# Performance work log

Hardware: AMD Instinct MI355X
Metric: run time of the kernel (lower is better)

## Reference

```python
import jax, jax.numpy as jnp
import numpy as np

D_MODEL = 1024


def pos_encoding(seq_len, d_model):
    # pos: [S,1], i: [d/2]
    pos = jnp.arange(seq_len, dtype=jnp.float32)[:, None]
    i = jnp.arange(0, d_model, 2, dtype=jnp.float32)
    angle_rates = 1.0 / jnp.power(10000.0, i / d_model)
    angle_rads = pos * angle_rates  # [S, d/2]
    # NOTE: original concatenates sin block then cos block (not interleaved)
    return jnp.concatenate([jnp.sin(angle_rads), jnp.cos(angle_rads)], axis=-1)  # [S, d]


def setup_inputs() -> dict:
    key = jax.random.key(0)
    ks = jax.random.split(key, 4)
    B, S, D = 4, 2048, D_MODEL
    scale = 1.0 / np.sqrt(D)
    x = jax.random.normal(ks[0], (B, S, D), dtype=jnp.float32)
    Wq = jax.random.normal(ks[1], (D, D), dtype=jnp.float32) * scale
    Wk = jax.random.normal(ks[2], (D, D), dtype=jnp.float32) * scale
    Wv = jax.random.normal(ks[3], (D, D), dtype=jnp.float32) * scale
    bq = jnp.zeros((D,), dtype=jnp.float32)
    bk = jnp.zeros((D,), dtype=jnp.float32)
    bv = jnp.zeros((D,), dtype=jnp.float32)
    return {"x": x, "Wq": Wq, "bq": bq, "Wk": Wk, "bk": bk, "Wv": Wv, "bv": bv}


def reference(x, Wq, bq, Wk, bk, Wv, bv):
    B, S, D = x.shape
    pe = pos_encoding(S, D)  # [S, D]
    h = x + pe[None, :, :]
    q = jnp.einsum('bsd,de->bse', h, Wq) + bq
    k = jnp.einsum('bsd,de->bse', h, Wk) + bk
    v = jnp.einsum('bsd,de->bse', h, Wv) + bv
    logits = jnp.einsum('bqd,bkd->bqk', q, k) / jnp.sqrt(jnp.float32(D))
    attn = jax.nn.softmax(logits, axis=-1)
    out = jnp.einsum('bqk,bkd->bqd', attn, v)
    return x + out
```

## Files before the change

kernel.cpp:

```cpp
#include <hip/hip_runtime.h>
#include <stdint.h>


#define AS1(p) ((__attribute__((address_space(1))) void*)(p))
#define AS3(p) ((__attribute__((address_space(3))) void*)(p))

typedef _Float16 f16x8 __attribute__((ext_vector_type(8)));
typedef _Float16 f16x4 __attribute__((ext_vector_type(4)));
typedef float f32x4 __attribute__((ext_vector_type(4)));

__global__ __launch_bounds__(256) void prep(const float* __restrict__ x,
                                            _Float16* __restrict__ h,
                                            const float* __restrict__ Wq,
                                            const float* __restrict__ Wk,
                                            const float* __restrict__ Wv,
                                            _Float16* __restrict__ Wt,
                                            float* __restrict__ rowsum) {
  const int bx = blockIdx.x;
  const int tid = threadIdx.x;
  if (bx < 8192) {
    const size_t e = ((size_t)bx * 256 + tid) * 4;
    const int d = (int)(e & 1023);
    const int s = (int)((e >> 10) & 2047);
    const float4 xv = *(const float4*)(x + e);
    const int half = d >> 9;
    const int j0 = d & 511;
    const float c = -0.017988946039016f;
    f16x4 o;
#pragma unroll
    for (int t = 0; t < 4; t++) {
      const float r = __expf((float)(j0 + t) * c);
      const float a = (float)s * r;
      const float p = half ? __cosf(a) : __sinf(a);
      const float xe = (t == 0) ? xv.x : (t == 1) ? xv.y : (t == 2) ? xv.z : xv.w;
      o[t] = (_Float16)(xe + p);
    }
    *(f16x4*)(h + e) = o;
  } else if (bx < 11264) {
    __shared__ float t[32][33];
    const int w = bx - 8192;
    const int z = w >> 10;
    const int rem = w & 1023;
    const int n0 = (rem & 31) * 32, k0 = (rem >> 5) * 32;
    const float* W = (z == 0) ? Wq : (z == 1) ? Wk : Wv;
    _Float16* o = Wt + (size_t)z * 1048576;
    const int tx = tid & 31, ty = tid >> 5;
#pragma unroll
    for (int i = ty; i < 32; i += 8)
      t[i][tx] = W[(size_t)(k0 + i) * 1024 + (n0 + tx)];
    __syncthreads();
#pragma unroll
    for (int i = ty; i < 32; i += 8)
      o[(size_t)(n0 + i) * 1024 + (k0 + tx)] = (_Float16)t[tx][i];
  } else {
    rowsum[(bx - 11264) * 256 + tid] = 0.f;
  }
}

template <int MODE>
__global__ __launch_bounds__(512) void gemm8p(
    const _Float16* __restrict__ A0, long long sA,
    const _Float16* __restrict__ B0, long long sB,
    void* __restrict__ C0, long long sC,
    const float* __restrict__ aux0, const float* __restrict__ aux1,
    const float* __restrict__ aux2, float* __restrict__ rowsum,
    _Float16* __restrict__ vT, const int K, const int N, const int ldc) {
  __shared__ __align__(16) _Float16 As[2][2][8192];
  __shared__ __align__(16) _Float16 Bs[2][2][8192];
  const int tid = threadIdx.x;
  const int bid = blockIdx.x;

  int z, bm0, bn0;
  if (MODE == 0) {
    const int w = (bid & 7) * 48 + (bid >> 3);
    const int m = w / 12, r = w - m * 12;
    z = r >> 2; bn0 = (r & 3) * 256; bm0 = m * 256;
  } else {
    const int w = (bid & 7) * 32 + (bid >> 3);
    z = w >> 6;
    const int r = w & 63;
    bm0 = (r >> 3) * 256; bn0 = (r & 7) * 256;
  }
  const _Float16* A = A0 + (size_t)z * sA;
  const _Float16* Bt = B0 + (size_t)z * sB;

  const _Float16* aS = A + (size_t)(bm0 + (tid >> 2)) * K + (tid & 3) * 8;
  const _Float16* bS = Bt + (size_t)(bn0 + (tid >> 2)) * K + (tid & 3) * 8;
  const size_t half = (size_t)128 * K;

  auto stage = [&](int kt, int q) {
    const int b = kt & 1;
    _Float16* ad = &As[b][q][tid * 8];
    _Float16* bd = &Bs[b][q][tid * 8];
    const _Float16* ag = aS + kt * 64 + q * 32;
    const _Float16* bg = bS + kt * 64 + q * 32;
    __builtin_amdgcn_global_load_lds(AS1(ag), AS3(ad), 16, 0, 0);
    __builtin_amdgcn_global_load_lds(AS1(ag + half), AS3(ad + 4096), 16, 0, 0);
    __builtin_amdgcn_global_load_lds(AS1(bg), AS3(bd), 16, 0, 0);
    __builtin_amdgcn_global_load_lds(AS1(bg + half), AS3(bd + 4096), 16, 0, 0);
  };

  const int lane = tid & 63, wave = tid >> 6;
  const int wr = wave >> 2, wc = wave & 3;
  const int quad = lane >> 4, l16 = lane & 15;

  f32x4 acc[8][4];
#pragma unroll
  for (int i = 0; i < 8; i++)
#pragma unroll
    for (int j = 0; j < 4; j++) {
      f32x4 zz = {0.f, 0.f, 0.f, 0.f};
      acc[i][j] = zz;
    }

  const int nt = K >> 6;

  stage(0, 0); stage(0, 1); stage(1, 0);
  asm volatile("s_waitcnt vmcnt(8)" ::: "memory");
  __builtin_amdgcn_s_barrier();

  for (int t = 0; t < nt; ++t) {
    const int b = t & 1;
#pragma unroll
    for (int q = 0; q < 2; ++q) {
      f16x8 af[8], bf[4];
#pragma unroll
      for (int i = 0; i < 8; i++)
        af[i] = *(const f16x8*)&As[b][q][(wr * 128 + i * 16 + l16) * 32 + quad * 8];
#pragma unroll
      for (int j = 0; j < 4; j++)
        bf[j] = *(const f16x8*)&Bs[b][q][(wc * 64 + j * 16 + l16) * 32 + quad * 8];
      if (q == 0) { if (t + 1 < nt) stage(t + 1, 1); }
      else        { if (t + 2 < nt) stage(t + 2, 0); }
      __builtin_amdgcn_s_barrier();
      asm volatile("s_waitcnt lgkmcnt(0)" ::: "memory");
      __builtin_amdgcn_sched_barrier(0);
      __builtin_amdgcn_s_setprio(1);
#pragma unroll
      for (int i = 0; i < 8; i++)
#pragma unroll
        for (int j = 0; j < 4; j++)
          acc[i][j] = __builtin_amdgcn_mfma_f32_16x16x32_f16(af[i], bf[j],
                                                             acc[i][j], 0, 0, 0);
      __builtin_amdgcn_s_setprio(0);
      __builtin_amdgcn_sched_barrier(0);
      const bool last = (t == nt - 1) && (q == 1);
      if (!last) {
        if (q == 0) {
          if (t + 1 < nt) asm volatile("s_waitcnt vmcnt(8)" ::: "memory");
          else            asm volatile("s_waitcnt vmcnt(0)" ::: "memory");
        } else {
          if (t + 3 <= nt) asm volatile("s_waitcnt vmcnt(8)" ::: "memory");
          else             asm volatile("s_waitcnt vmcnt(4)" ::: "memory");
        }
        __builtin_amdgcn_s_barrier();
      }
    }
  }

  const int rowb = bm0 + wr * 128 + quad * 4;
  const int colb = bn0 + wc * 64 + l16;
  if (MODE == 0) {
    const float* bias = (z == 0) ? aux0 : (z == 1) ? aux1 : aux2;
    if (z == 2) {
      const int bb_ = rowb >> 11, sl = rowb & 2047;
      _Float16* vb = vT + (size_t)bb_ * 2097152;
#pragma unroll
      for (int i = 0; i < 8; i++)
#pragma unroll
        for (int j = 0; j < 4; j++) {
          const int gn = colb + j * 16;
          const float bb = bias[gn];
          f16x4 o;
#pragma unroll
          for (int r = 0; r < 4; r++) o[r] = (_Float16)(acc[i][j][r] + bb);
          *(f16x4*)&vb[(size_t)gn * 2048 + sl + i * 16] = o;
        }
    } else {
      _Float16* C = (_Float16*)C0 + (size_t)z * sC;
#pragma unroll
      for (int i = 0; i < 8; i++)
#pragma unroll
        for (int j = 0; j < 4; j++) {
          const int gn = colb + j * 16;
          const float bb = bias[gn];
#pragma unroll
          for (int r = 0; r < 4; r++)
            C[(size_t)(rowb + i * 16 + r) * N + gn] = (_Float16)(acc[i][j][r] + bb);
        }
    }
  } else {
    _Float16* C = (_Float16*)C0 + (size_t)z * sC;
    float rs[4] = {0.f, 0.f, 0.f, 0.f};
#pragma unroll
    for (int i = 0; i < 8; i++)
#pragma unroll
      for (int j = 0; j < 4; j++) {
        const int gn = colb + j * 16;
        f16x4 o;
        float pj = 0.f;
#pragma unroll
        for (int r = 0; r < 4; r++) {
          const float e = __expf(acc[i][j][r] * 0.03125f);
          o[r] = (_Float16)e;
          pj += e;
        }
        rs[j] += pj;
        *(f16x4*)&C[(size_t)gn * ldc + rowb + i * 16] = o;
      }
#pragma unroll
    for (int j = 0; j < 4; j++) {
      float v = rs[j];
      v += __shfl_xor(v, 16);
      v += __shfl_xor(v, 32);
      if (quad == 0) atomicAdd(&rowsum[z * 2048 + colb + j * 16], v);
    }
  }
}

__global__ __launch_bounds__(256) void gemm_pv(
    const _Float16* __restrict__ A0, long long sA,
    const _Float16* __restrict__ B0, long long sB,
    float* __restrict__ C0, long long sC,
    const float* __restrict__ X0, const float* __restrict__ rowsum,
    long long sX, const int K, const int ldc) {
  __shared__ __align__(16) _Float16 As[2 * 128 * 32];
  __shared__ __align__(16) _Float16 Bs[2 * 128 * 32];
  const int tid = threadIdx.x;
  const int bid = blockIdx.x;

  const int c = bid & 7, t0 = bid >> 3;
  const int zx = (t0 & 3) * 8 + c;
  const int y = t0 >> 2;
  const int z = zx >> 3;
  const int bm0 = (zx & 7) * 128, bn0 = y * 128;

  const _Float16* A = A0 + (size_t)z * sA;
  const _Float16* Bt = B0 + (size_t)z * sB;

  const _Float16* a0 = A + (size_t)(bm0 + (tid >> 2)) * K + (tid & 3) * 8;
  const _Float16* a1 = a0 + (size_t)64 * K;
  const _Float16* b0 = Bt + (size_t)(bn0 + (tid >> 2)) * K + (tid & 3) * 8;
  const _Float16* b1 = b0 + (size_t)64 * K;

  const int lane = tid & 63, wave = tid >> 6;
  const int wr = wave >> 1, wc = wave & 1;
  const int quad = lane >> 4, l16 = lane & 15;

  f32x4 acc[4][4];
#pragma unroll
  for (int i = 0; i < 4; i++)
#pragma unroll
    for (int j = 0; j < 4; j++) {
      f32x4 zz = {0.f, 0.f, 0.f, 0.f};
      acc[i][j] = zz;
    }

  for (int k0 = 0; k0 < K; k0 += 64) {
    __syncthreads();
#pragma unroll
    for (int u = 0; u < 2; u++) {
      __builtin_amdgcn_global_load_lds(AS1(a0 + k0 + u * 32),
                                       AS3(&As[u * 4096 + tid * 8]), 16, 0, 0);
      __builtin_amdgcn_global_load_lds(AS1(a1 + k0 + u * 32),
                                       AS3(&As[u * 4096 + tid * 8 + 2048]), 16, 0, 0);
      __builtin_amdgcn_global_load_lds(AS1(b0 + k0 + u * 32),
                                       AS3(&Bs[u * 4096 + tid * 8]), 16, 0, 0);
      __builtin_amdgcn_global_load_lds(AS1(b1 + k0 + u * 32),
                                       AS3(&Bs[u * 4096 + tid * 8 + 2048]), 16, 0, 0);
    }
    __syncthreads();
#pragma unroll
    for (int u = 0; u < 2; u++) {
      f16x8 af[4], bfr[4];
#pragma unroll
      for (int i = 0; i < 4; i++)
        af[i] = *(const f16x8*)&As[u * 4096 + (wr * 64 + i * 16 + l16) * 32 + quad * 8];
#pragma unroll
      for (int j = 0; j < 4; j++)
        bfr[j] = *(const f16x8*)&Bs[u * 4096 + (wc * 64 + j * 16 + l16) * 32 + quad * 8];
#pragma unroll
      for (int i = 0; i < 4; i++)
#pragma unroll
        for (int j = 0; j < 4; j++)
          acc[i][j] = __builtin_amdgcn_mfma_f32_16x16x32_f16(af[i], bfr[j],
                                                             acc[i][j], 0, 0, 0);
    }
  }

  const int rowb = bm0 + wr * 64 + quad * 4;
  const int colb = bn0 + wc * 64 + l16;
  float* C = C0 + (size_t)z * sC;
  const float* X = X0 + (size_t)z * sX;
  float inv[4];
#pragma unroll
  for (int j = 0; j < 4; j++)
    inv[j] = 1.0f / rowsum[z * 2048 + colb + j * 16];
#pragma unroll
  for (int i = 0; i < 4; i++)
#pragma unroll
    for (int j = 0; j < 4; j++) {
      const int gn = colb + j * 16;
      const size_t base = (size_t)gn * ldc + rowb + i * 16;
      const float4 xv = *(const float4*)(X + base);
      float4 o;
      o.x = acc[i][j][0] * inv[j] + xv.x;
      o.y = acc[i][j][1] * inv[j] + xv.y;
      o.z = acc[i][j][2] * inv[j] + xv.z;
      o.w = acc[i][j][3] * inv[j] + xv.w;
      *(float4*)(C + base) = o;
    }
}

extern "C" void kernel_launch(void* const* d_in, const int* in_sizes, int n_in,
                              void* d_out, int out_size, void* d_ws, size_t ws_size,
                              hipStream_t stream) {
  (void)in_sizes; (void)n_in; (void)out_size; (void)ws_size;
  const float* x  = (const float*)d_in[0];
  const float* Wq = (const float*)d_in[1];
  const float* bq = (const float*)d_in[2];
  const float* Wk = (const float*)d_in[3];
  const float* bk = (const float*)d_in[4];
  const float* Wv = (const float*)d_in[5];
  const float* bv = (const float*)d_in[6];
  float* out = (float*)d_out;
  char* ws = (char*)d_ws;

  _Float16* h    = (_Float16*)(ws);
  _Float16* Wt   = (_Float16*)(ws + 16777216);
  _Float16* qkv  = (_Float16*)(ws + 23068672);
  _Float16* attn = (_Float16*)(ws + 73400320);
  float* rowsum  = (float*)   (ws + 106954752);

  const long long E = 8388608;
  _Float16* vT = qkv + 2 * E;

  prep<<<11296, 256, 0, stream>>>(x, h, Wq, Wk, Wv, Wt, rowsum);

  gemm8p<0><<<384, 512, 0, stream>>>(
      h, 0LL, Wt, 1048576LL, qkv, E, bq, bk, bv, nullptr, vT,
      1024, 1024, 0);

  gemm8p<1><<<256, 512, 0, stream>>>(
      qkv + E, 2097152LL, qkv, 2097152LL, attn, 4194304LL,
      nullptr, nullptr, nullptr, rowsum, nullptr,
      1024, 2048, 2048);

  gemm_pv<<<512, 256, 0, stream>>>(
      vT, 2097152LL, attn, 4194304LL, out, 2097152LL,
      x, rowsum, 2097152LL, 2048, 1024);
}
```

Measured before the change: 271.8 us.

## Restructure GEMM main loops into finer-grained staged pipelines with quadrant MFMA phases

The 256x256 GEMM now loads full 64-wide K tiles per A/B half and splits each K step into four quadrant phases. Each phase issues a slice of the next prefetch between LDS fragment reads and MFMA bursts, so global loads are spread more evenly over the compute. The PV GEMM swaps its synchronous load-then-compute loop for a 4-slot ring buffer of 32-wide K stages, prefetched three stages ahead with vmcnt-based waits. This costs more LDS in the PV kernel and adds extra barriers per iteration in the main GEMM.

```diff
diff --git a/kernel.cpp b/kernel.cpp
--- a/kernel.cpp
+++ b/kernel.cpp
@@ -57,8 +57,39 @@
   }
 }
 
+#define RD_A(SET, S_)                                                         \
+  {                                                                           \
+    _Pragma("unroll") for (int fi = 0; fi < 4; fi++)                          \
+      _Pragma("unroll") for (int kk = 0; kk < 2; kk++)                        \
+        SET[fi * 2 + kk] = *(const f16x8*)&As[bb][kk][                        \
+            (wr * 128 + (S_) * 64 + fi * 16 + l16) * 32 + quad * 8];          \
+  }
+#define RD_B(SET, S_)                                                         \
+  {                                                                           \
+    _Pragma("unroll") for (int fj = 0; fj < 2; fj++)                          \
+      _Pragma("unroll") for (int kk = 0; kk < 2; kk++)                        \
+        SET[fj * 2 + kk] = *(const f16x8*)&Bs[bb][kk][                        \
+            (wc * 64 + (S_) * 32 + fj * 16 + l16) * 32 + quad * 8];           \
+  }
+#define MFMA16(ASET, BSET, MQ, NQ)                                            \
+  {                                                                           \
+    __builtin_amdgcn_s_setprio(1);                                            \
+    _Pragma("unroll") for (int fi = 0; fi < 4; fi++)                          \
+      _Pragma("unroll") for (int fj = 0; fj < 2; fj++)                        \
+        _Pragma("unroll") for (int kk = 0; kk < 2; kk++)                      \
+          acc[(MQ) * 4 + fi][(NQ) * 2 + fj] =                                 \
+              __builtin_amdgcn_mfma_f32_16x16x32_f16(                         \
+                  ASET[fi * 2 + kk], BSET[fj * 2 + kk],                       \
+                  acc[(MQ) * 4 + fi][(NQ) * 2 + fj], 0, 0, 0);                \
+    __builtin_amdgcn_s_setprio(0);                                            \
+  }
+#define PHASE_WAIT()                                                          \
+  __builtin_amdgcn_s_barrier();                                               \
+  asm volatile("s_waitcnt lgkmcnt(0)" ::: "memory");                          \
+  __builtin_amdgcn_sched_barrier(0);
+
 template <int MODE>
-__global__ __launch_bounds__(512) void gemm8p(
+__global__ __launch_bounds__(512) void gemm256(
     const _Float16* __restrict__ A0, long long sA,
     const _Float16* __restrict__ B0, long long sB,
     void* __restrict__ C0, long long sC,
@@ -86,18 +117,21 @@
 
   const _Float16* aS = A + (size_t)(bm0 + (tid >> 2)) * K + (tid & 3) * 8;
   const _Float16* bS = Bt + (size_t)(bn0 + (tid >> 2)) * K + (tid & 3) * 8;
-  const size_t half = (size_t)128 * K;
-
-  auto stage = [&](int kt, int q) {
-    const int b = kt & 1;
-    _Float16* ad = &As[b][q][tid * 8];
-    _Float16* bd = &Bs[b][q][tid * 8];
-    const _Float16* ag = aS + kt * 64 + q * 32;
-    const _Float16* bg = bS + kt * 64 + q * 32;
-    __builtin_amdgcn_global_load_lds(AS1(ag), AS3(ad), 16, 0, 0);
-    __builtin_amdgcn_global_load_lds(AS1(ag + half), AS3(ad + 4096), 16, 0, 0);
-    __builtin_amdgcn_global_load_lds(AS1(bg), AS3(bd), 16, 0, 0);
-    __builtin_amdgcn_global_load_lds(AS1(bg + half), AS3(bd + 4096), 16, 0, 0);
+  const size_t halfStep = (size_t)128 * K;
+
+  auto stageA = [&](int X, int h) {
+    const int b = X & 1;
+    const _Float16* s = aS + (size_t)X * 64 + (size_t)h * halfStep;
+    _Float16* d = &As[b][0][h * 4096 + tid * 8];
+    __builtin_amdgcn_global_load_lds(AS1(s), AS3(d), 16, 0, 0);
+    __builtin_amdgcn_global_load_lds(AS1(s + 32), AS3(d + 8192), 16, 0, 0);
+  };
+  auto stageB = [&](int X, int h) {
+    const int b = X & 1;
+    const _Float16* s = bS + (size_t)X * 64 + (size_t)h * halfStep;
+    _Float16* d = &Bs[b][0][h * 4096 + tid * 8];
+    __builtin_amdgcn_global_load_lds(AS1(s), AS3(d), 16, 0, 0);
+    __builtin_amdgcn_global_load_lds(AS1(s + 32), AS3(d + 8192), 16, 0, 0);
   };
 
   const int lane = tid & 63, wave = tid >> 6;
@@ -115,46 +149,38 @@
 
   const int nt = K >> 6;
 
-  stage(0, 0); stage(0, 1); stage(1, 0);
-  asm volatile("s_waitcnt vmcnt(8)" ::: "memory");
+  stageA(0, 0); stageA(0, 1); stageB(0, 0); stageB(0, 1);
+  stageA(1, 0); stageA(1, 1);
+  asm volatile("s_waitcnt vmcnt(4)" ::: "memory");
   __builtin_amdgcn_s_barrier();
 
-  for (int t = 0; t < nt; ++t) {
-    const int b = t & 1;
-#pragma unroll
-    for (int q = 0; q < 2; ++q) {
-      f16x8 af[8], bf[4];
-#pragma unroll
-      for (int i = 0; i < 8; i++)
-        af[i] = *(const f16x8*)&As[b][q][(wr * 128 + i * 16 + l16) * 32 + quad * 8];
-#pragma unroll
-      for (int j = 0; j < 4; j++)
-        bf[j] = *(const f16x8*)&Bs[b][q][(wc * 64 + j * 16 + l16) * 32 + quad * 8];
-      if (q == 0) { if (t + 1 < nt) stage(t + 1, 1); }
-      else        { if (t + 2 < nt) stage(t + 2, 0); }
+  f16x8 a0[8], a1[8], b0f[4], b1f[4];
+
+  for (int T = 0; T < nt; ++T) {
+    const int bb = T & 1;
+    RD_A(a0, 0);
+    RD_B(b0f, 0);
+    if (T + 1 < nt) stageB(T + 1, 0);
+    PHASE_WAIT();
+    MFMA16(a0, b0f, 0, 0);
+    __builtin_amdgcn_s_barrier();
+    RD_A(a1, 1);
+    if (T + 1 < nt) stageB(T + 1, 1);
+    PHASE_WAIT();
+    MFMA16(a1, b0f, 1, 0);
+    __builtin_amdgcn_s_barrier();
+    RD_B(b1f, 1);
+    if (T + 2 < nt) stageA(T + 2, 0);
+    PHASE_WAIT();
+    MFMA16(a0, b1f, 0, 1);
+    __builtin_amdgcn_s_barrier();
+    if (T + 2 < nt) stageA(T + 2, 1);
+    PHASE_WAIT();
+    MFMA16(a1, b1f, 1, 1);
+    if (T + 1 < nt) {
+      if (T + 2 < nt) asm volatile("s_waitcnt vmcnt(4)" ::: "memory");
+      else            asm volatile("s_waitcnt vmcnt(0)" ::: "memory");
       __builtin_amdgcn_s_barrier();
-      asm volatile("s_waitcnt lgkmcnt(0)" ::: "memory");
-      __builtin_amdgcn_sched_barrier(0);
-      __builtin_amdgcn_s_setprio(1);
-#pragma unroll
-      for (int i = 0; i < 8; i++)
-#pragma unroll
-        for (int j = 0; j < 4; j++)
-          acc[i][j] = __builtin_amdgcn_mfma_f32_16x16x32_f16(af[i], bf[j],
-                                                             acc[i][j], 0, 0, 0);
-      __builtin_amdgcn_s_setprio(0);
-      __builtin_amdgcn_sched_barrier(0);
-      const bool last = (t == nt - 1) && (q == 1);
-      if (!last) {
-        if (q == 0) {
-          if (t + 1 < nt) asm volatile("s_waitcnt vmcnt(8)" ::: "memory");
-          else            asm volatile("s_waitcnt vmcnt(0)" ::: "memory");
-        } else {
-          if (t + 3 <= nt) asm volatile("s_waitcnt vmcnt(8)" ::: "memory");
-          else             asm volatile("s_waitcnt vmcnt(4)" ::: "memory");
-        }
-        __builtin_amdgcn_s_barrier();
-      }
     }
   }
 
@@ -163,17 +189,17 @@
   if (MODE == 0) {
     const float* bias = (z == 0) ? aux0 : (z == 1) ? aux1 : aux2;
     if (z == 2) {
-      const int bb_ = rowb >> 11, sl = rowb & 2047;
-      _Float16* vb = vT + (size_t)bb_ * 2097152;
+      const int b_ = rowb >> 11, sl = rowb & 2047;
+      _Float16* vb = vT + (size_t)b_ * 2097152;
 #pragma unroll
       for (int i = 0; i < 8; i++)
 #pragma unroll
         for (int j = 0; j < 4; j++) {
           const int gn = colb + j * 16;
-          const float bb = bias[gn];
+          const float bb2 = bias[gn];
           f16x4 o;
 #pragma unroll
-          for (int r = 0; r < 4; r++) o[r] = (_Float16)(acc[i][j][r] + bb);
+          for (int r = 0; r < 4; r++) o[r] = (_Float16)(acc[i][j][r] + bb2);
           *(f16x4*)&vb[(size_t)gn * 2048 + sl + i * 16] = o;
         }
     } else {
@@ -183,10 +209,10 @@
 #pragma unroll
         for (int j = 0; j < 4; j++) {
           const int gn = colb + j * 16;
-          const float bb = bias[gn];
+          const float bb2 = bias[gn];
 #pragma unroll
           for (int r = 0; r < 4; r++)
-            C[(size_t)(rowb + i * 16 + r) * N + gn] = (_Float16)(acc[i][j][r] + bb);
+            C[(size_t)(rowb + i * 16 + r) * N + gn] = (_Float16)(acc[i][j][r] + bb2);
         }
     }
   } else {
@@ -224,8 +250,8 @@
     float* __restrict__ C0, long long sC,
     const float* __restrict__ X0, const float* __restrict__ rowsum,
     long long sX, const int K, const int ldc) {
-  __shared__ __align__(16) _Float16 As[2 * 128 * 32];
-  __shared__ __align__(16) _Float16 Bs[2 * 128 * 32];
+  __shared__ __align__(16) _Float16 As[4 * 4096];
+  __shared__ __align__(16) _Float16 Bs[4 * 4096];
   const int tid = threadIdx.x;
   const int bid = blockIdx.x;
 
@@ -243,6 +269,15 @@
   const _Float16* b0 = Bt + (size_t)(bn0 + (tid >> 2)) * K + (tid & 3) * 8;
   const _Float16* b1 = b0 + (size_t)64 * K;
 
+  auto stage = [&](int s) {
+    const int r = s & 3;
+    const int k = s * 32;
+    __builtin_amdgcn_global_load_lds(AS1(a0 + k), AS3(&As[r * 4096 + tid * 8]), 16, 0, 0);
+    __builtin_amdgcn_global_load_lds(AS1(a1 + k), AS3(&As[r * 4096 + tid * 8 + 2048]), 16, 0, 0);
+    __builtin_amdgcn_global_load_lds(AS1(b0 + k), AS3(&Bs[r * 4096 + tid * 8]), 16, 0, 0);
+    __builtin_amdgcn_global_load_lds(AS1(b1 + k), AS3(&Bs[r * 4096 + tid * 8 + 2048]), 16, 0, 0);
+  };
+
   const int lane = tid & 63, wave = tid >> 6;
   const int wr = wave >> 1, wc = wave & 1;
   const int quad = lane >> 4, l16 = lane & 15;
@@ -256,35 +291,39 @@
       acc[i][j] = zz;
     }
 
-  for (int k0 = 0; k0 < K; k0 += 64) {
-    __syncthreads();
-#pragma unroll
-    for (int u = 0; u < 2; u++) {
-      __builtin_amdgcn_global_load_lds(AS1(a0 + k0 + u * 32),
-                                       AS3(&As[u * 4096 + tid * 8]), 16, 0, 0);
-      __builtin_amdgcn_global_load_lds(AS1(a1 + k0 + u * 32),
-                                       AS3(&As[u * 4096 + tid * 8 + 2048]), 16, 0, 0);
-      __builtin_amdgcn_global_load_lds(AS1(b0 + k0 + u * 32),
-                                       AS3(&Bs[u * 4096 + tid * 8]), 16, 0, 0);
-      __builtin_amdgcn_global_load_lds(AS1(b1 + k0 + u * 32),
-                                       AS3(&Bs[u * 4096 + tid * 8 + 2048]), 16, 0, 0);
-    }
-    __syncthreads();
-#pragma unroll
-    for (int u = 0; u < 2; u++) {
-      f16x8 af[4], bfr[4];
-#pragma unroll
-      for (int i = 0; i < 4; i++)
-        af[i] = *(const f16x8*)&As[u * 4096 + (wr * 64 + i * 16 + l16) * 32 + quad * 8];
+  const int NS = K >> 5;
+
+  stage(0); stage(1); stage(2);
+  asm volatile("s_waitcnt vmcnt(8)" ::: "memory");
+  __builtin_amdgcn_s_barrier();
+
+  for (int s = 0; s < NS; ++s) {
+    const int r = s & 3;
+    f16x8 af[4], bf[4];
+#pragma unroll
+    for (int i = 0; i < 4; i++)
+      af[i] = *(const f16x8*)&As[r * 4096 + (wr * 64 + i * 16 + l16) * 32 + quad * 8];
+#pragma unroll
+    for (int j = 0; j < 4; j++)
+      bf[j] = *(const f16x8*)&Bs[r * 4096 + (wc * 64 + j * 16 + l16) * 32 + quad * 8];
+    if (s + 3 < NS) stage(s + 3);
+    __builtin_amdgcn_s_barrier();
+    asm volatile("s_waitcnt lgkmcnt(0)" ::: "memory");
+    __builtin_amdgcn_sched_barrier(0);
+    __builtin_amdgcn_s_setprio(1);
+#pragma unroll
+    for (int i = 0; i < 4; i++)
 #pragma unroll
       for (int j = 0; j < 4; j++)
-        bfr[j] = *(const f16x8*)&Bs[u * 4096 + (wc * 64 + j * 16 + l16) * 32 + quad * 8];
-#pragma unroll
-      for (int i = 0; i < 4; i++)
-#pragma unroll
-        for (int j = 0; j < 4; j++)
-          acc[i][j] = __builtin_amdgcn_mfma_f32_16x16x32_f16(af[i], bfr[j],
-                                                             acc[i][j], 0, 0, 0);
+        acc[i][j] = __builtin_amdgcn_mfma_f32_16x16x32_f16(af[i], bf[j],
+                                                           acc[i][j], 0, 0, 0);
+    __builtin_amdgcn_s_setprio(0);
+    __builtin_amdgcn_sched_barrier(0);
+    if (s + 1 < NS) {
+      if (s + 3 < NS)       asm volatile("s_waitcnt vmcnt(8)" ::: "memory");
+      else if (s + 3 == NS) asm volatile("s_waitcnt vmcnt(4)" ::: "memory");
+      else                  asm volatile("s_waitcnt vmcnt(0)" ::: "memory");
+      __builtin_amdgcn_s_barrier();
     }
   }
 
@@ -337,11 +376,11 @@
 
   prep<<<11296, 256, 0, stream>>>(x, h, Wq, Wk, Wv, Wt, rowsum);
 
-  gemm8p<0><<<384, 512, 0, stream>>>(
+  gemm256<0><<<384, 512, 0, stream>>>(
       h, 0LL, Wt, 1048576LL, qkv, E, bq, bk, bv, nullptr, vT,
       1024, 1024, 0);
 
-  gemm8p<1><<<256, 512, 0, stream>>>(
+  gemm256<1><<<256, 512, 0, stream>>>(
       qkv + E, 2097152LL, qkv, 2097152LL, attn, 4194304LL,
       nullptr, nullptr, nullptr, rowsum, nullptr,
       1024, 2048, 2048);
```

Measured after the change: 265.1 us. 1.03x faster.
